# Optimization experiments

Measured on AMD Instinct MI355X. Metric: run time of the kernel, lower is better.

The kernel has to match this reference:

```python
import jax, jax.numpy as jnp
import numpy as np
from jax import lax

L = 32          # lattice side
H = 128         # net_width / hidden_size
B = 512         # batch_size
EPS = 1e-8


def setup_inputs() -> dict:
    key = jax.random.key(0)
    k0, k1, k2, k3, k4 = jax.random.split(key, 5)
    # binary spin configurations in {0., 1.}
    samples = jnp.round(jax.random.uniform(k0, (B, L, L))).astype(jnp.float32)
    s1 = 1.0 / np.sqrt(H + 2)
    # per-cell linear1 weights: input = cat([x(2), h(H)]) -> H
    W1 = jax.random.uniform(k1, (L * L, H, H + 2), minval=-s1, maxval=s1, dtype=jnp.float32)
    b1 = jax.random.uniform(k2, (L * L, H), minval=-s1, maxval=s1, dtype=jnp.float32)
    sf = 1.0 / np.sqrt(H)
    # per-cell fc head: H -> 1
    Wf = jax.random.uniform(k3, (L * L, H), minval=-sf, maxval=sf, dtype=jnp.float32)
    bf = jax.random.uniform(k4, (L * L,), minval=-sf, maxval=sf, dtype=jnp.float32)
    return {"samples": samples, "W1": W1, "b1": b1, "Wf": Wf, "bf": bf}


def _log_prob(samples, W1, b1, Wf, bf):
    Bsz = samples.shape[0]
    dt = samples.dtype
    W1 = W1.reshape(L, L, H, H + 2)
    b1 = b1.reshape(L, L, H)
    Wf = Wf.reshape(L, L, H)
    bf = bf.reshape(L, L)

    rows = jnp.transpose(samples, (1, 0, 2))                       # (L, B, L)
    prev = jnp.concatenate([jnp.zeros((1, Bsz, L), dt), rows[:-1]], axis=0)  # row above (x_v); zeros for row 0
    parity = (jnp.arange(L) % 2) == 1                              # odd rows scan right-to-left (zigzag)

    def row_step(h_v, xs):
        cur, pv, p, Wr, br, wfr, bfr = xs
        # reorder everything into visitation order (reverse for odd rows)
        cur_o = jnp.where(p, cur[:, ::-1], cur)     # (B, L) current-row spins / mask
        pv_o = jnp.where(p, pv[:, ::-1], pv)        # (B, L) spins of row above (x_v)
        hv_o = jnp.where(p, h_v[::-1], h_v)         # (L, B, H) vertical hidden states
        Wr_o = jnp.where(p, Wr[::-1], Wr)
        br_o = jnp.where(p, br[::-1], br)
        wf_o = jnp.where(p, wfr[::-1], wfr)
        bf_o = jnp.where(p, bfr[::-1], bfr)
        # horizontal input x_h = previously visited spin in this row (0 at row start)
        xh = jnp.concatenate([jnp.zeros((Bsz, 1), dt), cur_o[:, :-1]], axis=1)  # (B, L)

        def cell(h_h, cxs):
            xh_j, xv_j, m_j, hv_j, W, b, wf, bfs = cxs
            xh_s = jnp.stack([xh_j, 1.0 - xh_j], axis=1)   # (B, 2)
            xv_s = jnp.stack([xv_j, 1.0 - xv_j], axis=1)   # (B, 2)
            # linear1 applied to both (x_h,h_h) and (x_v,h_v); linear2 is unused in the original forward
            inp = jnp.concatenate([xh_s, h_h], axis=1) + jnp.concatenate([xv_s, hv_j], axis=1)  # (B, H+2)
            h = jnp.tanh(inp @ W.T + 2.0 * b)              # (B, H)
            x_hat = jax.nn.sigmoid(h @ wf + bfs)           # (B,)
            lp = jnp.log(x_hat + EPS) * m_j + jnp.log(1.0 - x_hat + EPS) * (1.0 - m_j)
            return h, (h, lp)

        cxs = (xh.T, pv_o.T, cur_o.T, hv_o, Wr_o, br_o, wf_o, bf_o)
        _, (hs, lps) = lax.scan(cell, jnp.zeros((Bsz, H), dt), cxs)
        h_v_new = jnp.where(p, hs[::-1], hs)               # back to raw column order
        return h_v_new, lps.sum(axis=0)                    # (B,) row log-prob

    h_v0 = jnp.zeros((L, Bsz, H), dt)
    _, row_lps = lax.scan(row_step, h_v0, (rows, prev, parity, W1, b1, Wf, bf))
    return row_lps.sum(axis=0)                             # (B,)


def reference(samples, W1, b1, Wf, bf):
    return _log_prob(samples, W1, b1, Wf, bf)
```

## Files before the change

kernel.cpp:

```cpp
#include <hip/hip_runtime.h>
#include <math.h>
#include <stdint.h>

#define Lr 32
#define Hh 128
#define NCELL (Lr * Lr)
#define NEPS 1e-8f
#define CELLB 33792

typedef _Float16 f16;
typedef f16 h2 __attribute__((ext_vector_type(2)));
typedef uint32_t u32;
typedef u32 u32x4 __attribute__((ext_vector_type(4)));
typedef u32 u32x2 __attribute__((ext_vector_type(2)));

__device__ __forceinline__ void bar_lds() {
    asm volatile("s_waitcnt lgkmcnt(0)\n\ts_barrier" ::: "memory");
}

template<int CTRL>
__device__ __forceinline__ float dpp_get(float x) {
    return __int_as_float(__builtin_amdgcn_update_dpp(
        0, __float_as_int(x), CTRL, 0xf, 0xf, true));
}

__device__ __forceinline__ float rlane(float x, int l) {
    return __int_as_float(__builtin_amdgcn_readlane(__float_as_int(x), l));
}

__device__ __forceinline__ float dot2(h2 a, h2 b, float c) {
    return __builtin_amdgcn_fdot2(a, b, c, false);
}

__device__ __forceinline__ h2 bch2(u32 v) {
    union { u32 u; h2 h; } cv; cv.u = v; return cv.h;
}
__device__ __forceinline__ float h16(u32 w, int hi) {
    union { unsigned short u; f16 h; } c;
    c.u = (unsigned short)(hi ? (w >> 16) : (w & 0xffff));
    return (float)c.h;
}

__device__ __forceinline__ float fast_tanh(float x) {
    x = fminf(9.f, fmaxf(-9.f, x));
    const float e = __expf(2.f * x);
    return 1.f - 2.f / (e + 1.f);
}

__device__ __forceinline__ int cell_of(int s) {
    const int i = s >> 5, jj = s & 31;
    const int c = (i & 1) ? (Lr - 1 - jj) : jj;
    return i * Lr + c;
}

__global__ __launch_bounds__(256)
void transpose_w(const float* __restrict__ W1, const float* __restrict__ b1,
                 const float* __restrict__ Wf, char* __restrict__ Wt) {
    __shared__ float tile[Hh * 130];
    const int cell = blockIdx.x;
    const float* src = W1 + (size_t)cell * (Hh * 130);
    for (int idx = threadIdx.x; idx < Hh * 130; idx += 256)
        tile[idx] = src[idx];
    __syncthreads();
    char* dst = Wt + (size_t)cell * CELLB;
    const int t = threadIdx.x, kk = t >> 1, hf = t & 1;
    for (int q4 = 0; q4 < 8; ++q4) {
        union { u32x4 v; f16 h[8]; } o;
        for (int j = 0; j < 4; ++j) {
            const int p = hf * 32 + q4 * 4 + j;
            o.h[2 * j]     = (f16)tile[kk * 130 + 2 + 2 * p];
            o.h[2 * j + 1] = (f16)tile[kk * 130 + 3 + 2 * p];
        }
        *(u32x4*)(dst + q4 * 4096 + t * 16) = o.v;
    }
    if (t < Hh) {
        union { u32x2 v; f16 h[4]; } o;
        const float w0 = tile[t * 130 + 0], w1 = tile[t * 130 + 1];
        const float bb = 2.f * b1[cell * Hh + t];
        o.h[0] = (f16)(2.f * w1 + bb);
        o.h[1] = (f16)(w0 + w1 + bb);
        o.h[2] = (f16)(2.f * w0 + bb);
        o.h[3] = (f16)Wf[cell * Hh + t];
        *(u32x2*)(dst + 32768 + t * 8) = o.v;
    }
}

__global__ __launch_bounds__(256, 1)
void rnn2d(const float* __restrict__ samples,
           const char* __restrict__ Wt,
           const float* __restrict__ bfv,
           float* __restrict__ out)
{
    __shared__ __align__(16) h2  inp[2][2][64];
    __shared__ __align__(16) f16 hvh[2][Lr * Hh];
    __shared__ float smp2[2][NCELL];
    __shared__ float bfs[NCELL];
    __shared__ float fp_[2][2][4];
    __shared__ int   sidx[2][2];
    __shared__ float lpb[4];

    const int t    = threadIdx.x;
    const int k    = t >> 1;
    const int half = t & 1;
    const int w    = t >> 6;
    const int b0   = blockIdx.x * 2;

    u32 vc[8], vt;
    for (int q4 = 0; q4 < 8; ++q4) vc[q4] = (u32)(q4 * 4096 + t * 16);
    vt = (u32)(32768 + k * 8);

    {
        f16* z1 = (f16*)inp;
        for (int idx = t; idx < 2 * 2 * 64 * 2; idx += 256) z1[idx] = (f16)0.f;
        f16* z2 = (f16*)hvh;
        for (int idx = t; idx < 2 * Lr * Hh; idx += 256) z2[idx] = (f16)0.f;
        for (int idx = t; idx < NCELL; idx += 256) {
            smp2[0][idx] = samples[(size_t)b0 * NCELL + idx];
            smp2[1][idx] = samples[(size_t)(b0 + 1) * NCELL + idx];
            bfs[idx] = bfv[idx];
        }
        if (t == 0) { sidx[0][0] = 0; sidx[1][0] = 0; }
    }
    float lp = 0.f;

    u32x4 A0,A1,A2,A3,A4,A5,A6,A7, B0,B1,B2,B3,B4,B5,B6,B7;
    u32x4 C0,C1,C2,C3,C4,C5,C6,C7, D0,D1,D2,D3,D4,D5,D6,D7;
    u32x2 TA, TB, TC, TD;

#define ISSUE(S, W0,W1_,W2_,W3_,W4_,W5_,W6_,W7_, TT)                        \
    {                                                                       \
        const int s_ = ((S) < NCELL) ? (S) : 0;   \
        const char* cb_ = Wt + (size_t)cell_of(s_) * CELLB;                 \
        asm volatile("global_load_dwordx4 %0, %1, %2" : "=v"(W0)  : "v"(vc[0]), "s"(cb_)); \
        asm volatile("global_load_dwordx4 %0, %1, %2" : "=v"(W1_) : "v"(vc[1]), "s"(cb_)); \
        asm volatile("global_load_dwordx4 %0, %1, %2" : "=v"(W2_) : "v"(vc[2]), "s"(cb_)); \
        asm volatile("global_load_dwordx4 %0, %1, %2" : "=v"(W3_) : "v"(vc[3]), "s"(cb_)); \
        asm volatile("global_load_dwordx4 %0, %1, %2" : "=v"(W4_) : "v"(vc[4]), "s"(cb_)); \
        asm volatile("global_load_dwordx4 %0, %1, %2" : "=v"(W5_) : "v"(vc[5]), "s"(cb_)); \
        asm volatile("global_load_dwordx4 %0, %1, %2" : "=v"(W6_) : "v"(vc[6]), "s"(cb_)); \
        asm volatile("global_load_dwordx4 %0, %1, %2" : "=v"(W7_) : "v"(vc[7]), "s"(cb_)); \
        asm volatile("global_load_dwordx2 %0, %1, %2" : "=v"(TT)  : "v"(vt),    "s"(cb_)); \
    }

#define WAITP()                                                             \
    asm volatile("s_waitcnt vmcnt(18)" ::: "memory");                       \
    __builtin_amdgcn_sched_barrier(0);

#define DOT4(WQ, QQ, Q4)                                                    \
    {                                                                       \
        const u32x4 v_ = (WQ);                                              \
        const uint4 xa_ = *(const uint4*)&inp[0][QQ][half * 32 + (Q4) * 4]; \
        const uint4 xb_ = *(const uint4*)&inp[1][QQ][half * 32 + (Q4) * 4]; \
        a00 = dot2(bch2(v_.x), bch2(xa_.x), a00);                           \
        a10 = dot2(bch2(v_.x), bch2(xb_.x), a10);                           \
        a01 = dot2(bch2(v_.y), bch2(xa_.y), a01);                           \
        a11 = dot2(bch2(v_.y), bch2(xb_.y), a11);                           \
        a02 = dot2(bch2(v_.z), bch2(xa_.z), a02);                           \
        a12 = dot2(bch2(v_.z), bch2(xb_.z), a12);                           \
        a03 = dot2(bch2(v_.w), bch2(xa_.w), a03);                           \
        a13 = dot2(bch2(v_.w), bch2(xb_.w), a13);                           \
    }

#define PROC(S, Q, W0,W1_,W2_,W3_,W4_,W5_,W6_,W7_, TT)                      \
    {                                                                       \
        const int i_ = (S) >> 5, j_ = (S) & 31;                             \
        const int c_ = (i_ & 1) ? (Lr - 1 - j_) : j_;                       \
        const int sn_ = ((S) + 1 < NCELL) ? (S) + 1 : (S);                  \
        const int in_ = sn_ >> 5, jn_ = sn_ & 31;                           \
        const int cn_ = (in_ & 1) ? (Lr - 1 - jn_) : jn_;                   \
        const float hvn0 = (float)hvh[0][cn_ * Hh + k];                     \
        const float hvn1 = (float)hvh[1][cn_ * Hh + k];                     \
        \
        if (((t & 63) == 4) && (S) > 0) {                                   \
            const int e_ = w >> 1, r_ = w & 1;                              \
            const int cp_ = cell_of((S) - 1);                               \
            const float z_ = fp_[e_][Q][0] + fp_[e_][Q][1]                  \
                           + fp_[e_][Q][2] + fp_[e_][Q][3] + bfs[cp_];      \
            const float xh_ = 1.f / (1.f + __expf(-z_));                    \
            const float m_ = smp2[e_][cp_];                                 \
            lp += (r_ == 0) ? __logf(xh_ + NEPS) * m_                       \
                            : __logf(1.f - xh_ + NEPS) * (1.f - m_);        \
        }                                                                   \
        \
        float a00=0.f,a01=0.f,a02=0.f,a03=0.f;                              \
        float a10=0.f,a11=0.f,a12=0.f,a13=0.f;                              \
        DOT4(W0,  Q, 0) DOT4(W1_, Q, 1)                                     \
        DOT4(W2_, Q, 2) DOT4(W3_, Q, 3)                                     \
        DOT4(W4_, Q, 4) DOT4(W5_, Q, 5)                                     \
        DOT4(W6_, Q, 6) DOT4(W7_, Q, 7)                                     \
        \
        const int sx0 = sidx[0][Q], sx1 = sidx[1][Q];                       \
        const float t0_ = h16(TT.x, 0), t1_ = h16(TT.x, 1);                 \
        const float t2_ = h16(TT.y, 0), wfv = h16(TT.y, 1);                 \
        float sp0 = (sx0 == 2) ? t2_ : ((sx0 == 1) ? t1_ : t0_);            \
        float sp1 = (sx1 == 2) ? t2_ : ((sx1 == 1) ? t1_ : t0_);            \
        if (half) { sp0 = 0.f; sp1 = 0.f; }                                 \
        float s0 = ((a00 + a01) + (a02 + a03)) + sp0;                       \
        float s1 = ((a10 + a11) + (a12 + a13)) + sp1;                       \
        s0 += dpp_get<0xB1>(s0);    \
        s1 += dpp_get<0xB1>(s1);                                            \
        const float h0 = fast_tanh(s0);                                     \
        const float h1 = fast_tanh(s1);                                     \
         \
        float f0 = h0 * wfv, f1 = h1 * wfv;                                 \
        f0 += dpp_get<0x4E>(f0);  f1 += dpp_get<0x4E>(f1);                  \
        f0 += dpp_get<0x141>(f0); f1 += dpp_get<0x141>(f1);                 \
        f0 += dpp_get<0x140>(f0); f1 += dpp_get<0x140>(f1);                 \
        f0 = f0 + rlane(f0, 16) + rlane(f0, 32) + rlane(f0, 48);            \
        f1 = f1 + rlane(f1, 16) + rlane(f1, 32) + rlane(f1, 48);            \
        if ((S) + 1 < NCELL) {                                              \
            const float v0 = ((jn_ == 0) ? 0.f : h0)                        \
                           + ((cn_ == c_) ? h0 : hvn0);                     \
            const float v1 = ((jn_ == 0) ? 0.f : h1)                        \
                           + ((cn_ == c_) ? h1 : hvn1);                     \
            const float v0p = dpp_get<0x4E>(v0);     \
            const float v1p = dpp_get<0x4E>(v1);                            \
            if ((t & 3) == 0) {                                             \
                h2 u0; u0.x = (f16)v0; u0.y = (f16)v0p;                     \
                h2 u1; u1.x = (f16)v1; u1.y = (f16)v1p;                     \
                inp[0][(Q) ^ 1][t >> 2] = u0;                               \
                inp[1][(Q) ^ 1][t >> 2] = u1;                               \
            }                                                               \
            if (t == 0) {                                                   \
                const float xh0 = (jn_ == 0) ? 0.f : smp2[0][i_ * Lr + c_]; \
                const float xv0 = (in_ == 0) ? 0.f                          \
                                             : smp2[0][(in_ - 1) * Lr + cn_]; \
                const float xh1 = (jn_ == 0) ? 0.f : smp2[1][i_ * Lr + c_]; \
                const float xv1 = (in_ == 0) ? 0.f                          \
                                             : smp2[1][(in_ - 1) * Lr + cn_]; \
                sidx[0][(Q) ^ 1] = (int)(xh0 + xv0);                        \
                sidx[1][(Q) ^ 1] = (int)(xh1 + xv1);                        \
            }                                                               \
        }                                                                   \
        hvh[0][c_ * Hh + k] = (f16)h0;        \
        hvh[1][c_ * Hh + k] = (f16)h1;                                      \
        if ((t & 63) == 0) {                                                \
            fp_[0][(Q) ^ 1][w] = f0;                                        \
            fp_[1][(Q) ^ 1][w] = f1;                                        \
        }                                                                   \
        bar_lds();        \
    }

    ISSUE(0, A0,A1,A2,A3,A4,A5,A6,A7, TA);
    ISSUE(1, B0,B1,B2,B3,B4,B5,B6,B7, TB);
    __syncthreads();

    for (int s = 0; s < NCELL; s += 4) {
        ISSUE(s + 2, C0,C1,C2,C3,C4,C5,C6,C7, TC); WAITP();
        PROC(s,     0, A0,A1,A2,A3,A4,A5,A6,A7, TA);
        ISSUE(s + 3, D0,D1,D2,D3,D4,D5,D6,D7, TD); WAITP();
        PROC(s + 1, 1, B0,B1,B2,B3,B4,B5,B6,B7, TB);
        ISSUE(s + 4, A0,A1,A2,A3,A4,A5,A6,A7, TA); WAITP();
        PROC(s + 2, 0, C0,C1,C2,C3,C4,C5,C6,C7, TC);
        ISSUE(s + 5, B0,B1,B2,B3,B4,B5,B6,B7, TB); WAITP();
        PROC(s + 3, 1, D0,D1,D2,D3,D4,D5,D6,D7, TD);
    }
#undef ISSUE
#undef WAITP
#undef DOT4
#undef PROC

    if ((t & 63) == 4) {
        const int e_ = w >> 1, r_ = w & 1;
        const int cp_ = cell_of(NCELL - 1);
        const float z_ = fp_[e_][0][0] + fp_[e_][0][1]
                       + fp_[e_][0][2] + fp_[e_][0][3] + bfs[cp_];
        const float xh_ = 1.f / (1.f + __expf(-z_));
        const float m_ = smp2[e_][cp_];
        lp += (r_ == 0) ? __logf(xh_ + NEPS) * m_
                        : __logf(1.f - xh_ + NEPS) * (1.f - m_);
        lpb[w] = lp;
    }
    __syncthreads();
    if (t == 0) {
        out[b0]     = lpb[0] + lpb[1];
        out[b0 + 1] = lpb[2] + lpb[3];
    }
}

extern "C" void kernel_launch(void* const* d_in, const int* in_sizes, int n_in,
                              void* d_out, int out_size, void* d_ws, size_t ws_size,
                              hipStream_t stream) {
    const float* samples = (const float*)d_in[0];
    const float* W1      = (const float*)d_in[1];
    const float* b1      = (const float*)d_in[2];
    const float* Wf      = (const float*)d_in[3];
    const float* bf      = (const float*)d_in[4];
    float* outp = (float*)d_out;
    char* Wt = (char*)d_ws;

    transpose_w<<<1024, 256, 0, stream>>>(W1, b1, Wf, Wt);
    rnn2d<<<256, 256, 0, stream>>>(samples, Wt, bf, outp);
}
```

Baseline: 1.056 ms.

## Process one batch element per block and launch twice as many blocks

Each block now handles a single batch sample instead of two, with the per-sample LDS buffers, dot accumulators and reductions halved. The grid grows from 256 to 512 blocks and launch bounds allow two blocks per CU, so more blocks can run concurrently on the MI355X's CUs. The cost is that every weight tile streamed from global memory now serves one sample instead of two, doubling total weight traffic per cell, while the serial per-cell chain and barrier count per block stay the same.

```diff
diff --git a/kernel.cpp b/kernel.cpp
--- a/kernel.cpp
+++ b/kernel.cpp
@@ -85,25 +85,25 @@
     }
 }
 
-__global__ __launch_bounds__(256, 1)
+__global__ __launch_bounds__(256, 2)
 void rnn2d(const float* __restrict__ samples,
            const char* __restrict__ Wt,
            const float* __restrict__ bfv,
            float* __restrict__ out)
 {
-    __shared__ __align__(16) h2  inp[2][2][64];
-    __shared__ __align__(16) f16 hvh[2][Lr * Hh];
-    __shared__ float smp2[2][NCELL];
+    __shared__ __align__(16) h2  inp[2][64];
+    __shared__ __align__(16) f16 hvh[Lr * Hh];
+    __shared__ float smp[NCELL];
     __shared__ float bfs[NCELL];
-    __shared__ float fp_[2][2][4];
-    __shared__ int   sidx[2][2];
-    __shared__ float lpb[4];
+    __shared__ float fp_[2][4];
+    __shared__ int   sidx[2];
+    __shared__ float lpb[2];
 
     const int t    = threadIdx.x;
     const int k    = t >> 1;
     const int half = t & 1;
     const int w    = t >> 6;
-    const int b0   = blockIdx.x * 2;
+    const int b    = blockIdx.x;
 
     u32 vc[8], vt;
     for (int q4 = 0; q4 < 8; ++q4) vc[q4] = (u32)(q4 * 4096 + t * 16);
@@ -111,15 +111,14 @@
 
     {
         f16* z1 = (f16*)inp;
-        for (int idx = t; idx < 2 * 2 * 64 * 2; idx += 256) z1[idx] = (f16)0.f;
+        for (int idx = t; idx < 2 * 64 * 2; idx += 256) z1[idx] = (f16)0.f;
         f16* z2 = (f16*)hvh;
-        for (int idx = t; idx < 2 * Lr * Hh; idx += 256) z2[idx] = (f16)0.f;
+        for (int idx = t; idx < Lr * Hh; idx += 256) z2[idx] = (f16)0.f;
         for (int idx = t; idx < NCELL; idx += 256) {
-            smp2[0][idx] = samples[(size_t)b0 * NCELL + idx];
-            smp2[1][idx] = samples[(size_t)(b0 + 1) * NCELL + idx];
+            smp[idx] = samples[(size_t)b * NCELL + idx];
             bfs[idx] = bfv[idx];
         }
-        if (t == 0) { sidx[0][0] = 0; sidx[1][0] = 0; }
+        if (t == 0) sidx[0] = 0;
     }
     float lp = 0.f;
 
@@ -149,16 +148,11 @@
 #define DOT4(WQ, QQ, Q4)                                                    \
     {                                                                       \
         const u32x4 v_ = (WQ);                                              \
-        const uint4 xa_ = *(const uint4*)&inp[0][QQ][half * 32 + (Q4) * 4]; \
-        const uint4 xb_ = *(const uint4*)&inp[1][QQ][half * 32 + (Q4) * 4]; \
+        const uint4 xa_ = *(const uint4*)&inp[QQ][half * 32 + (Q4) * 4];    \
         a00 = dot2(bch2(v_.x), bch2(xa_.x), a00);                           \
-        a10 = dot2(bch2(v_.x), bch2(xb_.x), a10);                           \
         a01 = dot2(bch2(v_.y), bch2(xa_.y), a01);                           \
-        a11 = dot2(bch2(v_.y), bch2(xb_.y), a11);                           \
         a02 = dot2(bch2(v_.z), bch2(xa_.z), a02);                           \
-        a12 = dot2(bch2(v_.z), bch2(xb_.z), a12);                           \
         a03 = dot2(bch2(v_.w), bch2(xa_.w), a03);                           \
-        a13 = dot2(bch2(v_.w), bch2(xb_.w), a13);                           \
     }
 
 #define PROC(S, Q, W0,W1_,W2_,W3_,W4_,W5_,W6_,W7_, TT)                      \
@@ -168,76 +162,55 @@
         const int sn_ = ((S) + 1 < NCELL) ? (S) + 1 : (S);                  \
         const int in_ = sn_ >> 5, jn_ = sn_ & 31;                           \
         const int cn_ = (in_ & 1) ? (Lr - 1 - jn_) : jn_;                   \
-        const float hvn0 = (float)hvh[0][cn_ * Hh + k];                     \
-        const float hvn1 = (float)hvh[1][cn_ * Hh + k];                     \
+        const float hvn = (float)hvh[cn_ * Hh + k];                         \
         \
-        if (((t & 63) == 4) && (S) > 0) {                                   \
-            const int e_ = w >> 1, r_ = w & 1;                              \
+        if (((t & 63) == 4) && (w < 2) && (S) > 0) {                        \
             const int cp_ = cell_of((S) - 1);                               \
-            const float z_ = fp_[e_][Q][0] + fp_[e_][Q][1]                  \
-                           + fp_[e_][Q][2] + fp_[e_][Q][3] + bfs[cp_];      \
+            const float z_ = fp_[Q][0] + fp_[Q][1]                          \
+                           + fp_[Q][2] + fp_[Q][3] + bfs[cp_];              \
             const float xh_ = 1.f / (1.f + __expf(-z_));                    \
-            const float m_ = smp2[e_][cp_];                                 \
-            lp += (r_ == 0) ? __logf(xh_ + NEPS) * m_                       \
-                            : __logf(1.f - xh_ + NEPS) * (1.f - m_);        \
+            const float m_ = smp[cp_];                                      \
+            lp += (w == 0) ? __logf(xh_ + NEPS) * m_                        \
+                           : __logf(1.f - xh_ + NEPS) * (1.f - m_);         \
         }                                                                   \
         \
         float a00=0.f,a01=0.f,a02=0.f,a03=0.f;                              \
-        float a10=0.f,a11=0.f,a12=0.f,a13=0.f;                              \
         DOT4(W0,  Q, 0) DOT4(W1_, Q, 1)                                     \
         DOT4(W2_, Q, 2) DOT4(W3_, Q, 3)                                     \
         DOT4(W4_, Q, 4) DOT4(W5_, Q, 5)                                     \
         DOT4(W6_, Q, 6) DOT4(W7_, Q, 7)                                     \
         \
-        const int sx0 = sidx[0][Q], sx1 = sidx[1][Q];                       \
+        const int sx = sidx[Q];                                             \
         const float t0_ = h16(TT.x, 0), t1_ = h16(TT.x, 1);                 \
         const float t2_ = h16(TT.y, 0), wfv = h16(TT.y, 1);                 \
-        float sp0 = (sx0 == 2) ? t2_ : ((sx0 == 1) ? t1_ : t0_);            \
-        float sp1 = (sx1 == 2) ? t2_ : ((sx1 == 1) ? t1_ : t0_);            \
-        if (half) { sp0 = 0.f; sp1 = 0.f; }                                 \
-        float s0 = ((a00 + a01) + (a02 + a03)) + sp0;                       \
-        float s1 = ((a10 + a11) + (a12 + a13)) + sp1;                       \
+        float sp = (sx == 2) ? t2_ : ((sx == 1) ? t1_ : t0_);               \
+        if (half) sp = 0.f;                                                 \
+        float s0 = ((a00 + a01) + (a02 + a03)) + sp;                        \
         s0 += dpp_get<0xB1>(s0);    \
-        s1 += dpp_get<0xB1>(s1);                                            \
         const float h0 = fast_tanh(s0);                                     \
-        const float h1 = fast_tanh(s1);                                     \
          \
-        float f0 = h0 * wfv, f1 = h1 * wfv;                                 \
-        f0 += dpp_get<0x4E>(f0);  f1 += dpp_get<0x4E>(f1);                  \
-        f0 += dpp_get<0x141>(f0); f1 += dpp_get<0x141>(f1);                 \
-        f0 += dpp_get<0x140>(f0); f1 += dpp_get<0x140>(f1);                 \
+        float f0 = h0 * wfv;                                                \
+        f0 += dpp_get<0x4E>(f0);                                            \
+        f0 += dpp_get<0x141>(f0);                                           \
+        f0 += dpp_get<0x140>(f0);                                           \
         f0 = f0 + rlane(f0, 16) + rlane(f0, 32) + rlane(f0, 48);            \
-        f1 = f1 + rlane(f1, 16) + rlane(f1, 32) + rlane(f1, 48);            \
         if ((S) + 1 < NCELL) {                                              \
             const float v0 = ((jn_ == 0) ? 0.f : h0)                        \
-                           + ((cn_ == c_) ? h0 : hvn0);                     \
-            const float v1 = ((jn_ == 0) ? 0.f : h1)                        \
-                           + ((cn_ == c_) ? h1 : hvn1);                     \
+                           + ((cn_ == c_) ? h0 : hvn);                      \
             const float v0p = dpp_get<0x4E>(v0);     \
-            const float v1p = dpp_get<0x4E>(v1);                            \
             if ((t & 3) == 0) {                                             \
                 h2 u0; u0.x = (f16)v0; u0.y = (f16)v0p;                     \
-                h2 u1; u1.x = (f16)v1; u1.y = (f16)v1p;                     \
-                inp[0][(Q) ^ 1][t >> 2] = u0;                               \
-                inp[1][(Q) ^ 1][t >> 2] = u1;                               \
+                inp[(Q) ^ 1][t >> 2] = u0;                                  \
             }                                                               \
             if (t == 0) {                                                   \
-                const float xh0 = (jn_ == 0) ? 0.f : smp2[0][i_ * Lr + c_]; \
+                const float xh0 = (jn_ == 0) ? 0.f : smp[i_ * Lr + c_];     \
                 const float xv0 = (in_ == 0) ? 0.f                          \
-                                             : smp2[0][(in_ - 1) * Lr + cn_]; \
-                const float xh1 = (jn_ == 0) ? 0.f : smp2[1][i_ * Lr + c_]; \
-                const float xv1 = (in_ == 0) ? 0.f                          \
-                                             : smp2[1][(in_ - 1) * Lr + cn_]; \
-                sidx[0][(Q) ^ 1] = (int)(xh0 + xv0);                        \
-                sidx[1][(Q) ^ 1] = (int)(xh1 + xv1);                        \
+                                             : smp[(in_ - 1) * Lr + cn_];   \
+                sidx[(Q) ^ 1] = (int)(xh0 + xv0);                           \
             }                                                               \
         }                                                                   \
-        hvh[0][c_ * Hh + k] = (f16)h0;        \
-        hvh[1][c_ * Hh + k] = (f16)h1;                                      \
-        if ((t & 63) == 0) {                                                \
-            fp_[0][(Q) ^ 1][w] = f0;                                        \
-            fp_[1][(Q) ^ 1][w] = f1;                                        \
-        }                                                                   \
+        hvh[c_ * Hh + k] = (f16)h0;           \
+        if ((t & 63) == 0) fp_[(Q) ^ 1][w] = f0;                            \
         bar_lds();        \
     }
 
@@ -260,22 +233,18 @@
 #undef DOT4
 #undef PROC
 
-    if ((t & 63) == 4) {
-        const int e_ = w >> 1, r_ = w & 1;
+    if (((t & 63) == 4) && (w < 2)) {
         const int cp_ = cell_of(NCELL - 1);
-        const float z_ = fp_[e_][0][0] + fp_[e_][0][1]
-                       + fp_[e_][0][2] + fp_[e_][0][3] + bfs[cp_];
+        const float z_ = fp_[0][0] + fp_[0][1] + fp_[0][2] + fp_[0][3]
+                       + bfs[cp_];
         const float xh_ = 1.f / (1.f + __expf(-z_));
-        const float m_ = smp2[e_][cp_];
-        lp += (r_ == 0) ? __logf(xh_ + NEPS) * m_
-                        : __logf(1.f - xh_ + NEPS) * (1.f - m_);
+        const float m_ = smp[cp_];
+        lp += (w == 0) ? __logf(xh_ + NEPS) * m_
+                       : __logf(1.f - xh_ + NEPS) * (1.f - m_);
         lpb[w] = lp;
     }
     __syncthreads();
-    if (t == 0) {
-        out[b0]     = lpb[0] + lpb[1];
-        out[b0 + 1] = lpb[2] + lpb[3];
-    }
+    if (t == 0) out[b] = lpb[0] + lpb[1];
 }
 
 extern "C" void kernel_launch(void* const* d_in, const int* in_sizes, int n_in,
@@ -290,5 +259,5 @@
     char* Wt = (char*)d_ws;
 
     transpose_w<<<1024, 256, 0, stream>>>(W1, b1, Wf, Wt);
-    rnn2d<<<256, 256, 0, stream>>>(samples, Wt, bf, outp);
-}
+    rnn2d<<<512, 256, 0, stream>>>(samples, Wt, bf, outp);
+}
```

Result: faster. 960.4 us (-9.1%).
